# Kernel tuning notes

Measured on AMD Instinct MI355X. Metric: run time of the kernel, lower is better.

## Reference

```python
import jax, jax.numpy as jnp
import numpy as np

B, S, H, T = 32, 512, 256, 48
START_IDX, STOP_IDX = 46, 47
NEG = -10000.0


def setup_inputs() -> dict:
    key = jax.random.key(0)
    k1, k2, k3, k4, k5 = jax.random.split(key, 5)
    lstm_features = jax.random.normal(k1, (B, S, H), dtype=jnp.float32)
    emission_w = jax.random.normal(k2, (H, T), dtype=jnp.float32) * 0.02
    emission_b = jnp.zeros((T,), dtype=jnp.float32)
    transitions = jax.random.normal(k3, (T, T), dtype=jnp.float32)
    transitions = transitions.at[:, START_IDX].set(NEG).at[STOP_IDX, :].set(NEG)
    lengths = jax.random.randint(k4, (B,), S // 2, S + 1, dtype=jnp.int32)
    tags = jax.random.randint(k5, (B, S), 0, START_IDX, dtype=jnp.int32)
    return {
        'lstm_features': lstm_features,
        'emission_w': emission_w,
        'emission_b': emission_b,
        'transitions': transitions,
        'lengths': lengths,
        'tags': tags,
    }


def _crf_scores(lstm_features, emission_w, emission_b, transitions):
    # emission: [B,S,T] at the 'to' tag; crf[b,s,i,j] = emission[b,s,j] + transitions[i,j]
    em = jnp.einsum('bsh,ht->bst', lstm_features, emission_w) + emission_b
    return em[:, :, None, :] + transitions[None, None, :, :]


def _forward_alg(crf_scores, transitions, lengths):
    # alpha[b,j] = log-sum-exp over paths ending at tag j
    alpha0 = jnp.full((B, T), NEG, dtype=crf_scores.dtype).at[:, START_IDX].set(0.0)

    def step(alpha, xs):
        crf_t, t = xs  # crf_t: [B,T,T]
        tag_var = crf_t + alpha[:, :, None]  # add score of 'from' tag
        new_alpha = jax.scipy.special.logsumexp(tag_var, axis=1)  # reduce over 'from'
        alpha = jnp.where((t < lengths)[:, None], new_alpha, alpha)
        return alpha, None

    xs = (jnp.swapaxes(crf_scores, 0, 1), jnp.arange(S, dtype=lengths.dtype))
    alpha, _ = jax.lax.scan(step, alpha0, xs)
    terminal = alpha + transitions[:, STOP_IDX][None, :]
    return jax.scipy.special.logsumexp(terminal, axis=1)  # [B]


def _gold_score(crf_scores, transitions, tags, lengths):
    # from_tags[t] = START for t=0 else tags[t-1]; to_tags[t] = tags[t]
    start_col = jnp.full((B, 1), START_IDX, dtype=tags.dtype)
    from_tags = jnp.concatenate([start_col, tags[:, :-1]], axis=1)  # [B,S]
    b_idx = jnp.arange(B)[:, None]
    s_idx = jnp.arange(S)[None, :]
    sel = crf_scores[b_idx, s_idx, from_tags, tags]  # [B,S]
    mask = (s_idx < lengths[:, None]).astype(sel.dtype)
    last_tag = jnp.take_along_axis(tags, (lengths - 1)[:, None], axis=1)[:, 0]
    return jnp.sum(sel * mask, axis=1) + transitions[last_tag, STOP_IDX]  # [B]


def reference(lstm_features, emission_w, emission_b, transitions, lengths, tags):
    crf_scores = _crf_scores(lstm_features, emission_w, emission_b, transitions)
    all_paths = _forward_alg(crf_scores, transitions, lengths)
    gold = _gold_score(crf_scores, transitions, tags, lengths)
    return all_paths - gold  # per-example NLL, shape [B]
```

## Files before the change

### kernel.cpp

```cpp
#include <hip/hip_runtime.h>
#include <math.h>

#define BB 32
#define SS 512
#define HH 256
#define TT 48
#define START_IDX 46
#define STOP_IDX 47

typedef __attribute__((ext_vector_type(8))) short short8;
typedef __attribute__((ext_vector_type(4))) float floatx4;

__device__ __forceinline__ float rfl(float x) {
    return __int_as_float(__builtin_amdgcn_readfirstlane(__float_as_int(x)));
}
__device__ __forceinline__ unsigned int bf16_rne(float x) {
    const unsigned int u = __float_as_uint(x);
    return (u + 0x7fffu + ((u >> 16) & 1u)) >> 16;
}
__device__ __forceinline__ float bf2f(unsigned short h) {
    return __uint_as_float(((unsigned int)h) << 16);
}

__global__ __launch_bounds__(256) void emission_kernel(
    const float* __restrict__ f, const float* __restrict__ w,
    const float* __restrict__ bias, const float* __restrict__ trans,
    unsigned short* __restrict__ exem, uint4* __restrict__ Ebuf)
{
    __shared__ __align__(16) char smem[50176];
    __shared__ float biaslds[TT];
    unsigned short* wb = (unsigned short*)smem;
    uint4* fragbuf = (uint4*)(smem + 25600);
    float* fl = (float*)smem;

    const int tid = threadIdx.x;

    if (blockIdx.x == 0 && tid < 64) {
        const int g = tid >> 4, cl = tid & 15;
#pragma unroll
        for (int kc = 0; kc < 2; ++kc)
#pragma unroll
            for (int nt = 0; nt < 3; ++nt) {
                unsigned int p[4];
#pragma unroll
                for (int h2 = 0; h2 < 4; ++h2) {
                    const int k = kc * 32 + g * 8 + 2 * h2;
                    const int n = nt * 16 + cl;
                    const float lo = (k     < TT) ? __expf(trans[k * TT + n])       : 0.f;
                    const float hi = (k + 1 < TT) ? __expf(trans[(k + 1) * TT + n]) : 0.f;
                    p[h2] = bf16_rne(lo) | (bf16_rne(hi) << 16);
                }
                Ebuf[(kc * 3 + nt) * 64 + tid] = make_uint4(p[0], p[1], p[2], p[3]);
            }
    }

    for (int idx = tid; idx < HH * TT; idx += 256) {
        const int r = idx / TT;
        const int c = idx - r * TT;
        wb[r * 50 + c] = (unsigned short)bf16_rne(w[idx]);
    }
    if (tid < TT) biaslds[tid] = bias[tid];
    __syncthreads();

    for (int idx = tid; idx < 24 * 64; idx += 256) {
        const int fb = idx >> 6;
        const int l  = idx & 63;
        const int kt = fb / 3;
        const int nt = fb - kt * 3;
        const int kbase = kt * 32 + (l >> 4) * 8;
        const int col   = nt * 16 + (l & 15);
        unsigned int p[4];
#pragma unroll
        for (int h2 = 0; h2 < 4; ++h2) {
            const unsigned int lo = wb[(kbase + 2 * h2)     * 50 + col];
            const unsigned int hi = wb[(kbase + 2 * h2 + 1) * 50 + col];
            p[h2] = lo | (hi << 16);
        }
        fragbuf[idx] = make_uint4(p[0], p[1], p[2], p[3]);
    }
    __syncthreads();

    const int lane = tid & 63, wv = tid >> 6, g = lane >> 4, cl = lane & 15;

    short8 Bf[24];
#pragma unroll
    for (int fb = 0; fb < 24; ++fb)
        Bf[fb] = __builtin_bit_cast(short8, fragbuf[fb * 64 + lane]);
    __syncthreads();

    const int row0 = blockIdx.x * 64;
    floatx4 acc0 = {0.f,0.f,0.f,0.f}, acc1 = {0.f,0.f,0.f,0.f}, acc2 = {0.f,0.f,0.f,0.f};

    const int lr = wv * 16 + cl;
#pragma unroll
    for (int h = 0; h < 2; ++h) {
#pragma unroll
        for (int it = 0; it < 8; ++it) {
            const int idx = tid + it * 256;
            const int r = idx >> 5, k4 = idx & 31;
            const float4 v = ((const float4*)f)[(size_t)(row0 + r) * 64 + h * 32 + k4];
            *(float4*)&fl[r * 132 + k4 * 4] = v;
        }
        __syncthreads();
#pragma unroll
        for (int kt = 0; kt < 4; ++kt) {
            const float4 v0 = *(const float4*)&fl[lr * 132 + kt * 32 + g * 8];
            const float4 v1 = *(const float4*)&fl[lr * 132 + kt * 32 + g * 8 + 4];
            const unsigned int a0 = bf16_rne(v0.x) | (bf16_rne(v0.y) << 16);
            const unsigned int a1 = bf16_rne(v0.z) | (bf16_rne(v0.w) << 16);
            const unsigned int a2 = bf16_rne(v1.x) | (bf16_rne(v1.y) << 16);
            const unsigned int a3 = bf16_rne(v1.z) | (bf16_rne(v1.w) << 16);
            const short8 Af = __builtin_bit_cast(short8, make_uint4(a0, a1, a2, a3));
            const int kg = h * 4 + kt;
            acc0 = __builtin_amdgcn_mfma_f32_16x16x32_bf16(Af, Bf[kg * 3 + 0], acc0, 0, 0, 0);
            acc1 = __builtin_amdgcn_mfma_f32_16x16x32_bf16(Af, Bf[kg * 3 + 1], acc1, 0, 0, 0);
            acc2 = __builtin_amdgcn_mfma_f32_16x16x32_bf16(Af, Bf[kg * 3 + 2], acc2, 0, 0, 0);
        }
        __syncthreads();
    }

    const int outrow0 = row0 + wv * 16 + g * 4;
    const int n = cl;
#pragma unroll
    for (int r = 0; r < 4; ++r) {
        unsigned short* e = exem + (size_t)(outrow0 + r) * TT;
        e[ 0 + n] = (unsigned short)bf16_rne(__expf(acc0[r] + biaslds[ 0 + n]));
        e[16 + n] = (unsigned short)bf16_rne(__expf(acc1[r] + biaslds[16 + n]));
        e[32 + n] = (unsigned short)bf16_rne(__expf(acc2[r] + biaslds[32 + n]));
    }
}

__global__ __launch_bounds__(192) void chunk_kernel(
    const unsigned short* __restrict__ exem,
    const uint4* __restrict__ Ebuf,
    const int*   __restrict__ lengths,
    unsigned short* __restrict__ Qs,
    float* __restrict__ Ls3)
{
    __shared__ __align__(8)  unsigned short ebuf[16 * TT];
    __shared__ __align__(16) unsigned short abuf[3][17 * 56];

    const int bc = blockIdx.x, b = bc >> 5, c = bc & 31;
    const int len = lengths[b];
    int nsteps = (len - 1) - (c << 4);
    if (nsteps <= 0) return;
    if (nsteps > 16) nsteps = 16;

    const int tid = threadIdx.x;
    const int rb = tid >> 6, l = tid & 63, g = l >> 4, cl = l & 15;

    {
        const unsigned int* src = (const unsigned int*)(exem + ((size_t)b * SS + (c << 4)) * TT);
        unsigned int* dst = (unsigned int*)ebuf;
        dst[tid] = src[tid];
        dst[tid + 192] = src[tid + 192];
    }

    uint4 Bf[2][3];
#pragma unroll
    for (int kc = 0; kc < 2; ++kc)
#pragma unroll
        for (int nt = 0; nt < 3; ++nt)
            Bf[kc][nt] = Ebuf[(kc * 3 + nt) * 64 + l];

    __syncthreads();

    floatx4 acc[3];
#pragma unroll
    for (int nt = 0; nt < 3; ++nt)
#pragma unroll
        for (int r = 0; r < 4; ++r)
            acc[nt][r] = (16 * rb + 4 * g + r == nt * 16 + cl) ? 1.f : 0.f;

    float ev[3];
#pragma unroll
    for (int nt = 0; nt < 3; ++nt) ev[nt] = bf2f(ebuf[nt * 16 + cl]);

    float Lrb = 0.f;
    unsigned short* aw = abuf[rb];

    for (int s = 0; s < nsteps; ++s) {
        float scale = 1.f;
        if (s == 8) {
            const float sig = rfl(acc[0][0]);
            Lrb = __logf(sig);
            scale = __builtin_amdgcn_rcpf(sig);
        }
        const float f0 = ev[0] * scale, f1 = ev[1] * scale, f2 = ev[2] * scale;
#pragma unroll
        for (int r = 0; r < 4; ++r) {
            const int rw = (4 * g + r) * 56;
            aw[rw +      cl] = (unsigned short)bf16_rne(acc[0][r] * f0);
            aw[rw + 16 + cl] = (unsigned short)bf16_rne(acc[1][r] * f1);
            aw[rw + 32 + cl] = (unsigned short)bf16_rne(acc[2][r] * f2);
        }
        if (s + 1 < nsteps) {
#pragma unroll
            for (int nt = 0; nt < 3; ++nt)
                ev[nt] = bf2f(ebuf[(s + 1) * TT + nt * 16 + cl]);
        }
        uint4 a0 = *(const uint4*)&aw[cl * 56 + g * 8];
        uint4 a1 = *(const uint4*)&aw[cl * 56 + 32 + g * 8];
        if (g >= 2) a1 = make_uint4(0, 0, 0, 0);
        const floatx4 z = {0.f, 0.f, 0.f, 0.f};
#pragma unroll
        for (int nt = 0; nt < 3; ++nt) {
            floatx4 d = __builtin_amdgcn_mfma_f32_16x16x32_bf16(
                __builtin_bit_cast(short8, a0), __builtin_bit_cast(short8, Bf[0][nt]), z, 0, 0, 0);
            d = __builtin_amdgcn_mfma_f32_16x16x32_bf16(
                __builtin_bit_cast(short8, a1), __builtin_bit_cast(short8, Bf[1][nt]), d, 0, 0, 0);
            acc[nt] = d;
        }
    }

    unsigned short* qb = Qs + (size_t)bc * (TT * 64);
#pragma unroll
    for (int nt = 0; nt < 3; ++nt) {
        const unsigned int lo = bf16_rne(acc[nt][0]) | (bf16_rne(acc[nt][1]) << 16);
        const unsigned int hi = bf16_rne(acc[nt][2]) | (bf16_rne(acc[nt][3]) << 16);
        *(uint2*)&qb[(nt * 16 + cl) * 64 + 16 * rb + 4 * g] = make_uint2(lo, hi);
    }
    if (l == 0) Ls3[bc * 3 + rb] = Lrb;
}

__global__ __launch_bounds__(64) void finalize_kernel(
    const unsigned short* __restrict__ exem,
    const float* __restrict__ trans,
    const int*   __restrict__ lengths,
    const int*   __restrict__ tags,
    const unsigned short* __restrict__ Qs,
    const float* __restrict__ Ls3,
    float* __restrict__ out)
{
    __shared__ float tlds[TT * TT];
    __shared__ __align__(16) unsigned short vlds[64];
    __shared__ float Lsl[96];

    const int j = threadIdx.x, b = blockIdx.x, g = j >> 4, cl = j & 15;

    for (int idx = j; idx < TT * TT; idx += 64) tlds[idx] = trans[idx];

    const int len = lengths[b];
    const int nc = (len - 1 + 15) >> 4;
    for (int i = j; i < nc * 3; i += 64) Lsl[i] = Ls3[b * 96 + i];
    __builtin_amdgcn_wave_barrier();

    float gold = 0.f;
    for (int s = j; s < len; s += 64) {
        const int tag  = tags[b * SS + s];
        const int from = (s == 0) ? START_IDX : tags[b * SS + s - 1];
        gold += __logf(bf2f(exem[((size_t)b * SS + s) * TT + tag])) + tlds[from * TT + tag];
    }
    gold += __shfl_xor(gold, 32); gold += __shfl_xor(gold, 16); gold += __shfl_xor(gold, 8);
    gold += __shfl_xor(gold, 4);  gold += __shfl_xor(gold, 2);  gold += __shfl_xor(gold, 1);

    const float R0 = Lsl[0];
    float vj = 0.f;
    if (j < TT) vj = __expf(tlds[START_IDX * TT + j]) * __expf(Lsl[j >> 4] - R0);
    vlds[j] = (unsigned short)bf16_rne(vj);
    float L = R0;

    const unsigned short* qbase = Qs + (size_t)(b * 32) * (TT * 64);
    floatx4 accn[3];
    float inv = 1.f;

    uint4 pB0[3], pB1[3];
#pragma unroll
    for (int nt = 0; nt < 3; ++nt) {
        pB0[nt] = *(const uint4*)&qbase[(nt * 16 + cl) * 64 + g * 8];
        pB1[nt] = *(const uint4*)&qbase[(nt * 16 + cl) * 64 + 32 + g * 8];
    }

    for (int cc = 0; cc < nc; ++cc) {
        uint4 B0[3], B1[3];
#pragma unroll
        for (int nt = 0; nt < 3; ++nt) { B0[nt] = pB0[nt]; B1[nt] = pB1[nt]; }

        const int cn = (cc + 1 < nc) ? cc + 1 : cc;
#pragma unroll
        for (int nt = 0; nt < 3; ++nt) {
            pB0[nt] = *(const uint4*)&qbase[(size_t)cn * TT * 64 + (nt * 16 + cl) * 64 + g * 8];
            pB1[nt] = *(const uint4*)&qbase[(size_t)cn * TT * 64 + (nt * 16 + cl) * 64 + 32 + g * 8];
        }
#pragma unroll
        for (int nt = 0; nt < 3; ++nt)
            if (g >= 2) B1[nt] = make_uint4(0, 0, 0, 0);

        const uint4 A0 = *(const uint4*)&vlds[g * 8];
        const uint4 A1 = *(const uint4*)&vlds[32 + g * 8];

        const floatx4 z = {0.f, 0.f, 0.f, 0.f};
#pragma unroll
        for (int nt = 0; nt < 3; ++nt) {
            floatx4 d = __builtin_amdgcn_mfma_f32_16x16x32_bf16(
                __builtin_bit_cast(short8, A0), __builtin_bit_cast(short8, B0[nt]), z, 0, 0, 0);
            d = __builtin_amdgcn_mfma_f32_16x16x32_bf16(
                __builtin_bit_cast(short8, A1), __builtin_bit_cast(short8, B1[nt]), d, 0, 0, 0);
            accn[nt] = d;
        }

        const float sig = rfl(accn[0][0]);
        inv = __builtin_amdgcn_rcpf(sig);

        if (cc + 1 < nc) {
            const float Rn = Lsl[(cc + 1) * 3];
            const float fa0 = __expf(Lsl[(cc + 1) * 3 + 0] - Rn);
            const float fa1 = __expf(Lsl[(cc + 1) * 3 + 1] - Rn);
            const float fa2 = __expf(Lsl[(cc + 1) * 3 + 2] - Rn);
            L += __logf(sig) + Rn;
            if (j < 16) {
                vlds[ 0 + j] = (unsigned short)bf16_rne(accn[0][0] * inv * fa0);
                vlds[16 + j] = (unsigned short)bf16_rne(accn[1][0] * inv * fa1);
                vlds[32 + j] = (unsigned short)bf16_rne(accn[2][0] * inv * fa2);
            }
        } else {
            L += __logf(sig);
        }
    }

    float term = 0.f;
    if (j < 16) {
        const size_t erow = ((size_t)b * SS + (len - 1)) * TT;
#pragma unroll
        for (int nt = 0; nt < 3; ++nt) {
            const int col = nt * 16 + j;
            term += accn[nt][0] * inv * bf2f(exem[erow + col])
                    * __expf(tlds[col * TT + STOP_IDX]);
        }
    }
    term += __shfl_xor(term, 32); term += __shfl_xor(term, 16); term += __shfl_xor(term, 8);
    term += __shfl_xor(term, 4);  term += __shfl_xor(term, 2);  term += __shfl_xor(term, 1);

    if (j == 0) {
        const float all_paths = __logf(term) + L;
        const int last = tags[b * SS + len - 1];
        out[b] = all_paths - (gold + tlds[last * TT + STOP_IDX]);
    }
}

extern "C" void kernel_launch(void* const* d_in, const int* in_sizes, int n_in,
                              void* d_out, int out_size, void* d_ws, size_t ws_size,
                              hipStream_t stream) {
    const float* f       = (const float*)d_in[0];
    const float* w       = (const float*)d_in[1];
    const float* bias    = (const float*)d_in[2];
    const float* trans   = (const float*)d_in[3];
    const int*   lengths = (const int*)d_in[4];
    const int*   tags    = (const int*)d_in[5];
    float*       out     = (float*)d_out;

    char* ws = (char*)d_ws;
    unsigned short* exem = (unsigned short*)ws;
    unsigned short* Qs   = (unsigned short*)(ws + 1572864);
    float*          Lsc  = (float*)(ws + 7864320);
    uint4*          Ebuf = (uint4*)(ws + 7876608);

    emission_kernel<<<(BB * SS) / 64, 256, 0, stream>>>(f, w, bias, trans, exem, Ebuf);
    chunk_kernel<<<BB * 32, 192, 0, stream>>>(exem, Ebuf, lengths, Qs, Lsc);
    finalize_kernel<<<BB, 64, 0, stream>>>(exem, trans, lengths, tags, Qs, Lsc, out);
}
```

Baseline: 116.7 us.

## Fuse emission GEMM into chunk kernel and precompute finalize scale factors

Removes the separate emission kernel. Each chunk block now computes its own 16x48 emission tile with MFMA, reading features and weights straight from global memory and splitting the K dimension across its three waves, whose partial sums are reduced in LDS. Each block also builds its own exp(transitions) fragments. This drops one launch and the round trip through the workspace between kernels, at the cost of redundant weight and transition loads in every block. Finalize also precomputes the per-chunk exp scale factors into LDS instead of computing them inside the serial loop.

```diff
diff --git a/kernel.cpp b/kernel.cpp
--- a/kernel.cpp
+++ b/kernel.cpp
@@ -22,148 +22,100 @@
     return __uint_as_float(((unsigned int)h) << 16);
 }
 
-__global__ __launch_bounds__(256) void emission_kernel(
-    const float* __restrict__ f, const float* __restrict__ w,
-    const float* __restrict__ bias, const float* __restrict__ trans,
-    unsigned short* __restrict__ exem, uint4* __restrict__ Ebuf)
-{
-    __shared__ __align__(16) char smem[50176];
-    __shared__ float biaslds[TT];
-    unsigned short* wb = (unsigned short*)smem;
-    uint4* fragbuf = (uint4*)(smem + 25600);
-    float* fl = (float*)smem;
-
-    const int tid = threadIdx.x;
-
-    if (blockIdx.x == 0 && tid < 64) {
-        const int g = tid >> 4, cl = tid & 15;
-#pragma unroll
-        for (int kc = 0; kc < 2; ++kc)
-#pragma unroll
-            for (int nt = 0; nt < 3; ++nt) {
-                unsigned int p[4];
-#pragma unroll
-                for (int h2 = 0; h2 < 4; ++h2) {
-                    const int k = kc * 32 + g * 8 + 2 * h2;
-                    const int n = nt * 16 + cl;
-                    const float lo = (k     < TT) ? __expf(trans[k * TT + n])       : 0.f;
-                    const float hi = (k + 1 < TT) ? __expf(trans[(k + 1) * TT + n]) : 0.f;
-                    p[h2] = bf16_rne(lo) | (bf16_rne(hi) << 16);
-                }
-                Ebuf[(kc * 3 + nt) * 64 + tid] = make_uint4(p[0], p[1], p[2], p[3]);
-            }
-    }
-
-    for (int idx = tid; idx < HH * TT; idx += 256) {
-        const int r = idx / TT;
-        const int c = idx - r * TT;
-        wb[r * 50 + c] = (unsigned short)bf16_rne(w[idx]);
-    }
-    if (tid < TT) biaslds[tid] = bias[tid];
-    __syncthreads();
-
-    for (int idx = tid; idx < 24 * 64; idx += 256) {
-        const int fb = idx >> 6;
-        const int l  = idx & 63;
-        const int kt = fb / 3;
-        const int nt = fb - kt * 3;
-        const int kbase = kt * 32 + (l >> 4) * 8;
-        const int col   = nt * 16 + (l & 15);
-        unsigned int p[4];
-#pragma unroll
-        for (int h2 = 0; h2 < 4; ++h2) {
-            const unsigned int lo = wb[(kbase + 2 * h2)     * 50 + col];
-            const unsigned int hi = wb[(kbase + 2 * h2 + 1) * 50 + col];
-            p[h2] = lo | (hi << 16);
-        }
-        fragbuf[idx] = make_uint4(p[0], p[1], p[2], p[3]);
-    }
-    __syncthreads();
-
-    const int lane = tid & 63, wv = tid >> 6, g = lane >> 4, cl = lane & 15;
-
-    short8 Bf[24];
-#pragma unroll
-    for (int fb = 0; fb < 24; ++fb)
-        Bf[fb] = __builtin_bit_cast(short8, fragbuf[fb * 64 + lane]);
-    __syncthreads();
-
-    const int row0 = blockIdx.x * 64;
-    floatx4 acc0 = {0.f,0.f,0.f,0.f}, acc1 = {0.f,0.f,0.f,0.f}, acc2 = {0.f,0.f,0.f,0.f};
-
-    const int lr = wv * 16 + cl;
-#pragma unroll
-    for (int h = 0; h < 2; ++h) {
-#pragma unroll
-        for (int it = 0; it < 8; ++it) {
-            const int idx = tid + it * 256;
-            const int r = idx >> 5, k4 = idx & 31;
-            const float4 v = ((const float4*)f)[(size_t)(row0 + r) * 64 + h * 32 + k4];
-            *(float4*)&fl[r * 132 + k4 * 4] = v;
-        }
-        __syncthreads();
-#pragma unroll
-        for (int kt = 0; kt < 4; ++kt) {
-            const float4 v0 = *(const float4*)&fl[lr * 132 + kt * 32 + g * 8];
-            const float4 v1 = *(const float4*)&fl[lr * 132 + kt * 32 + g * 8 + 4];
-            const unsigned int a0 = bf16_rne(v0.x) | (bf16_rne(v0.y) << 16);
-            const unsigned int a1 = bf16_rne(v0.z) | (bf16_rne(v0.w) << 16);
-            const unsigned int a2 = bf16_rne(v1.x) | (bf16_rne(v1.y) << 16);
-            const unsigned int a3 = bf16_rne(v1.z) | (bf16_rne(v1.w) << 16);
-            const short8 Af = __builtin_bit_cast(short8, make_uint4(a0, a1, a2, a3));
-            const int kg = h * 4 + kt;
-            acc0 = __builtin_amdgcn_mfma_f32_16x16x32_bf16(Af, Bf[kg * 3 + 0], acc0, 0, 0, 0);
-            acc1 = __builtin_amdgcn_mfma_f32_16x16x32_bf16(Af, Bf[kg * 3 + 1], acc1, 0, 0, 0);
-            acc2 = __builtin_amdgcn_mfma_f32_16x16x32_bf16(Af, Bf[kg * 3 + 2], acc2, 0, 0, 0);
-        }
-        __syncthreads();
-    }
-
-    const int outrow0 = row0 + wv * 16 + g * 4;
-    const int n = cl;
-#pragma unroll
-    for (int r = 0; r < 4; ++r) {
-        unsigned short* e = exem + (size_t)(outrow0 + r) * TT;
-        e[ 0 + n] = (unsigned short)bf16_rne(__expf(acc0[r] + biaslds[ 0 + n]));
-        e[16 + n] = (unsigned short)bf16_rne(__expf(acc1[r] + biaslds[16 + n]));
-        e[32 + n] = (unsigned short)bf16_rne(__expf(acc2[r] + biaslds[32 + n]));
-    }
-}
-
-__global__ __launch_bounds__(192) void chunk_kernel(
-    const unsigned short* __restrict__ exem,
-    const uint4* __restrict__ Ebuf,
+__global__ __launch_bounds__(192) void chunk_fused_kernel(
+    const float* __restrict__ f,
+    const float* __restrict__ w,
+    const float* __restrict__ bias,
+    const float* __restrict__ trans,
     const int*   __restrict__ lengths,
+    unsigned short* __restrict__ exem,
     unsigned short* __restrict__ Qs,
     float* __restrict__ Ls3)
 {
-    __shared__ __align__(8)  unsigned short ebuf[16 * TT];
-    __shared__ __align__(16) unsigned short abuf[3][17 * 56];
+    __shared__ __align__(16) float elds[16 * TT];
+    __shared__ __align__(16) char scratch[9216];
+    float* pbuf = (float*)scratch;
+    unsigned short* abuf = (unsigned short*)scratch;
 
     const int bc = blockIdx.x, b = bc >> 5, c = bc & 31;
     const int len = lengths[b];
     int nsteps = (len - 1) - (c << 4);
-    if (nsteps <= 0) return;
     if (nsteps > 16) nsteps = 16;
 
     const int tid = threadIdx.x;
     const int rb = tid >> 6, l = tid & 63, g = l >> 4, cl = l & 15;
 
+    uint4 BfE[2][3];
+#pragma unroll
+    for (int kc = 0; kc < 2; ++kc)
+#pragma unroll
+        for (int nt = 0; nt < 3; ++nt) {
+            unsigned int p[4];
+#pragma unroll
+            for (int h = 0; h < 4; ++h) {
+                const int k = kc * 32 + g * 8 + 2 * h;
+                const int n = nt * 16 + cl;
+                const float lo = (k     < TT) ? __expf(trans[k * TT + n])       : 0.f;
+                const float hi = (k + 1 < TT) ? __expf(trans[(k + 1) * TT + n]) : 0.f;
+                p[h] = bf16_rne(lo) | (bf16_rne(hi) << 16);
+            }
+            BfE[kc][nt] = make_uint4(p[0], p[1], p[2], p[3]);
+        }
+
+    const int kt0 = rb * 3;
+    const int ktn = (rb < 2) ? 3 : 2;
+    const size_t grow = (size_t)(b * SS + c * 16 + cl);
+
+    floatx4 eacc[3] = {{0.f,0.f,0.f,0.f}, {0.f,0.f,0.f,0.f}, {0.f,0.f,0.f,0.f}};
+    for (int kk = 0; kk < ktn; ++kk) {
+        const int kt = kt0 + kk;
+        const float4 v0 = *(const float4*)(f + grow * HH + kt * 32 + g * 8);
+        const float4 v1 = *(const float4*)(f + grow * HH + kt * 32 + g * 8 + 4);
+        const unsigned int a0 = bf16_rne(v0.x) | (bf16_rne(v0.y) << 16);
+        const unsigned int a1 = bf16_rne(v0.z) | (bf16_rne(v0.w) << 16);
+        const unsigned int a2 = bf16_rne(v1.x) | (bf16_rne(v1.y) << 16);
+        const unsigned int a3 = bf16_rne(v1.z) | (bf16_rne(v1.w) << 16);
+        const short8 Af = __builtin_bit_cast(short8, make_uint4(a0, a1, a2, a3));
+#pragma unroll
+        for (int nt = 0; nt < 3; ++nt) {
+            unsigned int p[4];
+#pragma unroll
+            for (int h = 0; h < 4; ++h) {
+                const int k = kt * 32 + g * 8 + 2 * h;
+                const int n = nt * 16 + cl;
+                p[h] = bf16_rne(w[k * TT + n]) | (bf16_rne(w[(k + 1) * TT + n]) << 16);
+            }
+            eacc[nt] = __builtin_amdgcn_mfma_f32_16x16x32_bf16(
+                Af, __builtin_bit_cast(short8, make_uint4(p[0], p[1], p[2], p[3])),
+                eacc[nt], 0, 0, 0);
+        }
+    }
+#pragma unroll
+    for (int nt = 0; nt < 3; ++nt)
+#pragma unroll
+        for (int r = 0; r < 4; ++r)
+            pbuf[rb * 768 + (4 * g + r) * TT + nt * 16 + cl] = eacc[nt][r];
+    __syncthreads();
+
     {
-        const unsigned int* src = (const unsigned int*)(exem + ((size_t)b * SS + (c << 4)) * TT);
-        unsigned int* dst = (unsigned int*)ebuf;
-        dst[tid] = src[tid];
-        dst[tid + 192] = src[tid + 192];
-    }
-
-    uint4 Bf[2][3];
-#pragma unroll
-    for (int kc = 0; kc < 2; ++kc)
-#pragma unroll
-        for (int nt = 0; nt < 3; ++nt)
-            Bf[kc][nt] = Ebuf[(kc * 3 + nt) * 64 + l];
-
+        const int s  = tid / 12;
+        const int c0 = (tid - s * 12) * 4;
+        const float4 p0 = *(const float4*)&pbuf[       s * TT + c0];
+        const float4 p1 = *(const float4*)&pbuf[768  + s * TT + c0];
+        const float4 p2 = *(const float4*)&pbuf[1536 + s * TT + c0];
+        const float4 bv = *(const float4*)&bias[c0];
+        const float e0 = __expf(p0.x + p1.x + p2.x + bv.x);
+        const float e1 = __expf(p0.y + p1.y + p2.y + bv.y);
+        const float e2 = __expf(p0.z + p1.z + p2.z + bv.z);
+        const float e3 = __expf(p0.w + p1.w + p2.w + bv.w);
+        *(float4*)&elds[s * TT + c0] = make_float4(e0, e1, e2, e3);
+        const unsigned int lo = bf16_rne(e0) | (bf16_rne(e1) << 16);
+        const unsigned int hi = bf16_rne(e2) | (bf16_rne(e3) << 16);
+        *(uint2*)&exem[((size_t)(b * SS + c * 16 + s)) * TT + c0] = make_uint2(lo, hi);
+    }
     __syncthreads();
+
+    if (nsteps <= 0) return;
 
     floatx4 acc[3];
 #pragma unroll
@@ -174,10 +126,10 @@
 
     float ev[3];
 #pragma unroll
-    for (int nt = 0; nt < 3; ++nt) ev[nt] = bf2f(ebuf[nt * 16 + cl]);
+    for (int nt = 0; nt < 3; ++nt) ev[nt] = elds[nt * 16 + cl];
 
     float Lrb = 0.f;
-    unsigned short* aw = abuf[rb];
+    unsigned short* aw = abuf + rb * (17 * 56);
 
     for (int s = 0; s < nsteps; ++s) {
         float scale = 1.f;
@@ -197,7 +149,7 @@
         if (s + 1 < nsteps) {
 #pragma unroll
             for (int nt = 0; nt < 3; ++nt)
-                ev[nt] = bf2f(ebuf[(s + 1) * TT + nt * 16 + cl]);
+                ev[nt] = elds[(s + 1) * TT + nt * 16 + cl];
         }
         uint4 a0 = *(const uint4*)&aw[cl * 56 + g * 8];
         uint4 a1 = *(const uint4*)&aw[cl * 56 + 32 + g * 8];
@@ -206,9 +158,9 @@
 #pragma unroll
         for (int nt = 0; nt < 3; ++nt) {
             floatx4 d = __builtin_amdgcn_mfma_f32_16x16x32_bf16(
-                __builtin_bit_cast(short8, a0), __builtin_bit_cast(short8, Bf[0][nt]), z, 0, 0, 0);
+                __builtin_bit_cast(short8, a0), __builtin_bit_cast(short8, BfE[0][nt]), z, 0, 0, 0);
             d = __builtin_amdgcn_mfma_f32_16x16x32_bf16(
-                __builtin_bit_cast(short8, a1), __builtin_bit_cast(short8, Bf[1][nt]), d, 0, 0, 0);
+                __builtin_bit_cast(short8, a1), __builtin_bit_cast(short8, BfE[1][nt]), d, 0, 0, 0);
             acc[nt] = d;
         }
     }
@@ -235,6 +187,7 @@
     __shared__ float tlds[TT * TT];
     __shared__ __align__(16) unsigned short vlds[64];
     __shared__ float Lsl[96];
+    __shared__ float falds[96];
 
     const int j = threadIdx.x, b = blockIdx.x, g = j >> 4, cl = j & 15;
 
@@ -243,6 +196,9 @@
     const int len = lengths[b];
     const int nc = (len - 1 + 15) >> 4;
     for (int i = j; i < nc * 3; i += 64) Lsl[i] = Ls3[b * 96 + i];
+    __builtin_amdgcn_wave_barrier();
+    for (int i = j; i < nc * 3; i += 64)
+        falds[i] = __expf(Lsl[i] - Lsl[(i / 3) * 3]);
     __builtin_amdgcn_wave_barrier();
 
     float gold = 0.f;
@@ -256,7 +212,7 @@
 
     const float R0 = Lsl[0];
     float vj = 0.f;
-    if (j < TT) vj = __expf(tlds[START_IDX * TT + j]) * __expf(Lsl[j >> 4] - R0);
+    if (j < TT) vj = __expf(tlds[START_IDX * TT + j]) * falds[j >> 4];
     vlds[j] = (unsigned short)bf16_rne(vj);
     float L = R0;
 
@@ -303,13 +259,12 @@
         inv = __builtin_amdgcn_rcpf(sig);
 
         if (cc + 1 < nc) {
-            const float Rn = Lsl[(cc + 1) * 3];
-            const float fa0 = __expf(Lsl[(cc + 1) * 3 + 0] - Rn);
-            const float fa1 = __expf(Lsl[(cc + 1) * 3 + 1] - Rn);
-            const float fa2 = __expf(Lsl[(cc + 1) * 3 + 2] - Rn);
+            const float Rn  = Lsl[(cc + 1) * 3];
+            const float fa1 = falds[(cc + 1) * 3 + 1];
+            const float fa2 = falds[(cc + 1) * 3 + 2];
             L += __logf(sig) + Rn;
             if (j < 16) {
-                vlds[ 0 + j] = (unsigned short)bf16_rne(accn[0][0] * inv * fa0);
+                vlds[ 0 + j] = (unsigned short)bf16_rne(accn[0][0] * inv);
                 vlds[16 + j] = (unsigned short)bf16_rne(accn[1][0] * inv * fa1);
                 vlds[32 + j] = (unsigned short)bf16_rne(accn[2][0] * inv * fa2);
             }
@@ -353,9 +308,8 @@
     unsigned short* exem = (unsigned short*)ws;
     unsigned short* Qs   = (unsigned short*)(ws + 1572864);
     float*          Lsc  = (float*)(ws + 7864320);
-    uint4*          Ebuf = (uint4*)(ws + 7876608);
-
-    emission_kernel<<<(BB * SS) / 64, 256, 0, stream>>>(f, w, bias, trans, exem, Ebuf);
-    chunk_kernel<<<BB * 32, 192, 0, stream>>>(exem, Ebuf, lengths, Qs, Lsc);
+
+    chunk_fused_kernel<<<BB * 32, 192, 0, stream>>>(f, w, bias, trans, lengths,
+                                                    exem, Qs, Lsc);
     finalize_kernel<<<BB, 64, 0, stream>>>(exem, trans, lengths, tags, Qs, Lsc, out);
 }
```

Measured after the change: 121.8 us. 4.3% more time.

## Fuse chunk and finalize kernels via per-batch atomic last-block counter

Applied to the files above, without the earlier changes.

Merges the chunk-product kernel and the finalize kernel into one launch. Each block increments a per-batch atomic counter after a threadfence, and the last of the 32 chunk blocks for that batch runs the finalize sequence with one wave. Chunk blocks with no work no longer exit early so that they still increment the counter. Chunk rescale factors are precomputed once into shared memory, which removes exp calls from the serial chunk loop. This saves one kernel launch and the gap between kernels, at the cost of an extra memset launch, fence and atomic overhead, and larger shared memory use per block that may lower occupancy.

```diff
diff --git a/kernel.cpp b/kernel.cpp
--- a/kernel.cpp
+++ b/kernel.cpp
@@ -130,123 +130,127 @@
     }
 }
 
-__global__ __launch_bounds__(192) void chunk_kernel(
+__global__ __launch_bounds__(192) void chunk_finalize_kernel(
     const unsigned short* __restrict__ exem,
     const uint4* __restrict__ Ebuf,
+    const float* __restrict__ trans,
     const int*   __restrict__ lengths,
+    const int*   __restrict__ tags,
     unsigned short* __restrict__ Qs,
-    float* __restrict__ Ls3)
+    float* __restrict__ Ls3,
+    int*   __restrict__ cnt,
+    float* __restrict__ out)
 {
     __shared__ __align__(8)  unsigned short ebuf[16 * TT];
     __shared__ __align__(16) unsigned short abuf[3][17 * 56];
+    __shared__ int lastflag;
+    __shared__ float tlds[TT * TT];
+    __shared__ __align__(16) unsigned short vlds[64];
+    __shared__ float Lsl[96];
+    __shared__ float falds[96];
 
     const int bc = blockIdx.x, b = bc >> 5, c = bc & 31;
     const int len = lengths[b];
     int nsteps = (len - 1) - (c << 4);
-    if (nsteps <= 0) return;
     if (nsteps > 16) nsteps = 16;
 
     const int tid = threadIdx.x;
     const int rb = tid >> 6, l = tid & 63, g = l >> 4, cl = l & 15;
 
-    {
-        const unsigned int* src = (const unsigned int*)(exem + ((size_t)b * SS + (c << 4)) * TT);
-        unsigned int* dst = (unsigned int*)ebuf;
-        dst[tid] = src[tid];
-        dst[tid + 192] = src[tid + 192];
-    }
-
-    uint4 Bf[2][3];
-#pragma unroll
-    for (int kc = 0; kc < 2; ++kc)
+    if (nsteps > 0) {
+        {
+            const unsigned int* src = (const unsigned int*)(exem + ((size_t)b * SS + (c << 4)) * TT);
+            unsigned int* dst = (unsigned int*)ebuf;
+            dst[tid] = src[tid];
+            dst[tid + 192] = src[tid + 192];
+        }
+        uint4 Bf[2][3];
+#pragma unroll
+        for (int kc = 0; kc < 2; ++kc)
+#pragma unroll
+            for (int nt = 0; nt < 3; ++nt)
+                Bf[kc][nt] = Ebuf[(kc * 3 + nt) * 64 + l];
+        __syncthreads();
+
+        floatx4 acc[3];
 #pragma unroll
         for (int nt = 0; nt < 3; ++nt)
-            Bf[kc][nt] = Ebuf[(kc * 3 + nt) * 64 + l];
-
+#pragma unroll
+            for (int r = 0; r < 4; ++r)
+                acc[nt][r] = (16 * rb + 4 * g + r == nt * 16 + cl) ? 1.f : 0.f;
+
+        float ev[3];
+#pragma unroll
+        for (int nt = 0; nt < 3; ++nt) ev[nt] = bf2f(ebuf[nt * 16 + cl]);
+
+        float Lrb = 0.f;
+        unsigned short* aw = abuf[rb];
+
+        for (int s = 0; s < nsteps; ++s) {
+            float scale = 1.f;
+            if (s == 8) {
+                const float sig = rfl(acc[0][0]);
+                Lrb = __logf(sig);
+                scale = __builtin_amdgcn_rcpf(sig);
+            }
+            const float f0 = ev[0] * scale, f1 = ev[1] * scale, f2 = ev[2] * scale;
+#pragma unroll
+            for (int r = 0; r < 4; ++r) {
+                const int rw = (4 * g + r) * 56;
+                aw[rw +      cl] = (unsigned short)bf16_rne(acc[0][r] * f0);
+                aw[rw + 16 + cl] = (unsigned short)bf16_rne(acc[1][r] * f1);
+                aw[rw + 32 + cl] = (unsigned short)bf16_rne(acc[2][r] * f2);
+            }
+            if (s + 1 < nsteps) {
+#pragma unroll
+                for (int nt = 0; nt < 3; ++nt)
+                    ev[nt] = bf2f(ebuf[(s + 1) * TT + nt * 16 + cl]);
+            }
+            uint4 a0 = *(const uint4*)&aw[cl * 56 + g * 8];
+            uint4 a1 = *(const uint4*)&aw[cl * 56 + 32 + g * 8];
+            if (g >= 2) a1 = make_uint4(0, 0, 0, 0);
+            const floatx4 z = {0.f, 0.f, 0.f, 0.f};
+#pragma unroll
+            for (int nt = 0; nt < 3; ++nt) {
+                floatx4 d = __builtin_amdgcn_mfma_f32_16x16x32_bf16(
+                    __builtin_bit_cast(short8, a0), __builtin_bit_cast(short8, Bf[0][nt]), z, 0, 0, 0);
+                d = __builtin_amdgcn_mfma_f32_16x16x32_bf16(
+                    __builtin_bit_cast(short8, a1), __builtin_bit_cast(short8, Bf[1][nt]), d, 0, 0, 0);
+                acc[nt] = d;
+            }
+        }
+
+        unsigned short* qb = Qs + (size_t)bc * (TT * 64);
+#pragma unroll
+        for (int nt = 0; nt < 3; ++nt) {
+            const unsigned int lo = bf16_rne(acc[nt][0]) | (bf16_rne(acc[nt][1]) << 16);
+            const unsigned int hi = bf16_rne(acc[nt][2]) | (bf16_rne(acc[nt][3]) << 16);
+            *(uint2*)&qb[(nt * 16 + cl) * 64 + 16 * rb + 4 * g] = make_uint2(lo, hi);
+        }
+        if (l == 0) Ls3[bc * 3 + rb] = Lrb;
+    }
+
+    __threadfence();
+    if (tid == 0) {
+        const int old = atomicAdd(&cnt[b], 1);
+        lastflag = (old == 31);
+    }
     __syncthreads();
-
-    floatx4 acc[3];
-#pragma unroll
-    for (int nt = 0; nt < 3; ++nt)
-#pragma unroll
-        for (int r = 0; r < 4; ++r)
-            acc[nt][r] = (16 * rb + 4 * g + r == nt * 16 + cl) ? 1.f : 0.f;
-
-    float ev[3];
-#pragma unroll
-    for (int nt = 0; nt < 3; ++nt) ev[nt] = bf2f(ebuf[nt * 16 + cl]);
-
-    float Lrb = 0.f;
-    unsigned short* aw = abuf[rb];
-
-    for (int s = 0; s < nsteps; ++s) {
-        float scale = 1.f;
-        if (s == 8) {
-            const float sig = rfl(acc[0][0]);
-            Lrb = __logf(sig);
-            scale = __builtin_amdgcn_rcpf(sig);
-        }
-        const float f0 = ev[0] * scale, f1 = ev[1] * scale, f2 = ev[2] * scale;
-#pragma unroll
-        for (int r = 0; r < 4; ++r) {
-            const int rw = (4 * g + r) * 56;
-            aw[rw +      cl] = (unsigned short)bf16_rne(acc[0][r] * f0);
-            aw[rw + 16 + cl] = (unsigned short)bf16_rne(acc[1][r] * f1);
-            aw[rw + 32 + cl] = (unsigned short)bf16_rne(acc[2][r] * f2);
-        }
-        if (s + 1 < nsteps) {
-#pragma unroll
-            for (int nt = 0; nt < 3; ++nt)
-                ev[nt] = bf2f(ebuf[(s + 1) * TT + nt * 16 + cl]);
-        }
-        uint4 a0 = *(const uint4*)&aw[cl * 56 + g * 8];
-        uint4 a1 = *(const uint4*)&aw[cl * 56 + 32 + g * 8];
-        if (g >= 2) a1 = make_uint4(0, 0, 0, 0);
-        const floatx4 z = {0.f, 0.f, 0.f, 0.f};
-#pragma unroll
-        for (int nt = 0; nt < 3; ++nt) {
-            floatx4 d = __builtin_amdgcn_mfma_f32_16x16x32_bf16(
-                __builtin_bit_cast(short8, a0), __builtin_bit_cast(short8, Bf[0][nt]), z, 0, 0, 0);
-            d = __builtin_amdgcn_mfma_f32_16x16x32_bf16(
-                __builtin_bit_cast(short8, a1), __builtin_bit_cast(short8, Bf[1][nt]), d, 0, 0, 0);
-            acc[nt] = d;
-        }
-    }
-
-    unsigned short* qb = Qs + (size_t)bc * (TT * 64);
-#pragma unroll
-    for (int nt = 0; nt < 3; ++nt) {
-        const unsigned int lo = bf16_rne(acc[nt][0]) | (bf16_rne(acc[nt][1]) << 16);
-        const unsigned int hi = bf16_rne(acc[nt][2]) | (bf16_rne(acc[nt][3]) << 16);
-        *(uint2*)&qb[(nt * 16 + cl) * 64 + 16 * rb + 4 * g] = make_uint2(lo, hi);
-    }
-    if (l == 0) Ls3[bc * 3 + rb] = Lrb;
-}
-
-__global__ __launch_bounds__(64) void finalize_kernel(
-    const unsigned short* __restrict__ exem,
-    const float* __restrict__ trans,
-    const int*   __restrict__ lengths,
-    const int*   __restrict__ tags,
-    const unsigned short* __restrict__ Qs,
-    const float* __restrict__ Ls3,
-    float* __restrict__ out)
-{
-    __shared__ float tlds[TT * TT];
-    __shared__ __align__(16) unsigned short vlds[64];
-    __shared__ float Lsl[96];
-
-    const int j = threadIdx.x, b = blockIdx.x, g = j >> 4, cl = j & 15;
-
-    for (int idx = j; idx < TT * TT; idx += 64) tlds[idx] = trans[idx];
-
-    const int len = lengths[b];
+    if (!lastflag) return;
+    __threadfence();
+    if (tid >= 64) return;
+
+    for (int idx = l; idx < TT * TT; idx += 64) tlds[idx] = trans[idx];
+
     const int nc = (len - 1 + 15) >> 4;
-    for (int i = j; i < nc * 3; i += 64) Lsl[i] = Ls3[b * 96 + i];
+    for (int i = l; i < nc * 3; i += 64) Lsl[i] = Ls3[b * 96 + i];
     __builtin_amdgcn_wave_barrier();
+    for (int i = l; i < nc * 3; i += 64)
+        falds[i] = __expf(Lsl[i] - Lsl[(i / 3) * 3]);
+    __builtin_amdgcn_wave_barrier();
 
     float gold = 0.f;
-    for (int s = j; s < len; s += 64) {
+    for (int s = l; s < len; s += 64) {
         const int tag  = tags[b * SS + s];
         const int from = (s == 0) ? START_IDX : tags[b * SS + s - 1];
         gold += __logf(bf2f(exem[((size_t)b * SS + s) * TT + tag])) + tlds[from * TT + tag];
@@ -256,8 +260,8 @@
 
     const float R0 = Lsl[0];
     float vj = 0.f;
-    if (j < TT) vj = __expf(tlds[START_IDX * TT + j]) * __expf(Lsl[j >> 4] - R0);
-    vlds[j] = (unsigned short)bf16_rne(vj);
+    if (l < TT) vj = __expf(tlds[START_IDX * TT + l]) * falds[l >> 4];
+    vlds[l] = (unsigned short)bf16_rne(vj);
     float L = R0;
 
     const unsigned short* qbase = Qs + (size_t)(b * 32) * (TT * 64);
@@ -303,15 +307,14 @@
         inv = __builtin_amdgcn_rcpf(sig);
 
         if (cc + 1 < nc) {
-            const float Rn = Lsl[(cc + 1) * 3];
-            const float fa0 = __expf(Lsl[(cc + 1) * 3 + 0] - Rn);
-            const float fa1 = __expf(Lsl[(cc + 1) * 3 + 1] - Rn);
-            const float fa2 = __expf(Lsl[(cc + 1) * 3 + 2] - Rn);
+            const float Rn  = Lsl[(cc + 1) * 3];
+            const float fa1 = falds[(cc + 1) * 3 + 1];
+            const float fa2 = falds[(cc + 1) * 3 + 2];
             L += __logf(sig) + Rn;
-            if (j < 16) {
-                vlds[ 0 + j] = (unsigned short)bf16_rne(accn[0][0] * inv * fa0);
-                vlds[16 + j] = (unsigned short)bf16_rne(accn[1][0] * inv * fa1);
-                vlds[32 + j] = (unsigned short)bf16_rne(accn[2][0] * inv * fa2);
+            if (l < 16) {
+                vlds[ 0 + l] = (unsigned short)bf16_rne(accn[0][0] * inv);
+                vlds[16 + l] = (unsigned short)bf16_rne(accn[1][0] * inv * fa1);
+                vlds[32 + l] = (unsigned short)bf16_rne(accn[2][0] * inv * fa2);
             }
         } else {
             L += __logf(sig);
@@ -319,11 +322,11 @@
     }
 
     float term = 0.f;
-    if (j < 16) {
+    if (l < 16) {
         const size_t erow = ((size_t)b * SS + (len - 1)) * TT;
 #pragma unroll
         for (int nt = 0; nt < 3; ++nt) {
-            const int col = nt * 16 + j;
+            const int col = nt * 16 + l;
             term += accn[nt][0] * inv * bf2f(exem[erow + col])
                     * __expf(tlds[col * TT + STOP_IDX]);
         }
@@ -331,7 +334,7 @@
     term += __shfl_xor(term, 32); term += __shfl_xor(term, 16); term += __shfl_xor(term, 8);
     term += __shfl_xor(term, 4);  term += __shfl_xor(term, 2);  term += __shfl_xor(term, 1);
 
-    if (j == 0) {
+    if (l == 0) {
         const float all_paths = __logf(term) + L;
         const int last = tags[b * SS + len - 1];
         out[b] = all_paths - (gold + tlds[last * TT + STOP_IDX]);
@@ -354,8 +357,10 @@
     unsigned short* Qs   = (unsigned short*)(ws + 1572864);
     float*          Lsc  = (float*)(ws + 7864320);
     uint4*          Ebuf = (uint4*)(ws + 7876608);
-
+    int*            cnt  = (int*)(ws + 7882752);
+
+    hipMemsetAsync(cnt, 0, BB * sizeof(int), stream);
     emission_kernel<<<(BB * SS) / 64, 256, 0, stream>>>(f, w, bias, trans, exem, Ebuf);
-    chunk_kernel<<<BB * 32, 192, 0, stream>>>(exem, Ebuf, lengths, Qs, Lsc);
-    finalize_kernel<<<BB, 64, 0, stream>>>(exem, trans, lengths, tags, Qs, Lsc, out);
-}
+    chunk_finalize_kernel<<<BB * 32, 192, 0, stream>>>(exem, Ebuf, trans, lengths, tags,
+                                                       Qs, Lsc, cnt, out);
+}
```

New measurement: 199.6 us. 1.71x slower.
